# Performance work log

Measured on AMD Instinct MI355X. Metric: run time of the kernel, lower is better.

Reference implementation:

```python
import jax, jax.numpy as jnp
import numpy as np

HEADS = 16
DIM_HEAD = 64

def setup_inputs() -> dict:
    key = jax.random.key(0)
    k1, k2, k3 = jax.random.split(key, 3)
    B, F, N, DIM = 4, 16, 196, 1024
    ntok = 1 + F * N  # cls + frames*patches
    x = jax.random.normal(k1, (B, ntok, DIM), dtype=jnp.float32)
    w_qkv = jax.random.normal(k2, (DIM, 3 * HEADS * DIM_HEAD), dtype=jnp.float32) * (DIM ** -0.5)
    w_out = jax.random.normal(k3, (HEADS * DIM_HEAD, DIM), dtype=jnp.float32) * ((HEADS * DIM_HEAD) ** -0.5)
    return {"x": x, "w_qkv": w_qkv, "w_out": w_out, "f": F}

def _attn(q, k, v):
    # q: [b, i, d], k/v: [b, j, d]
    sim = jnp.einsum('bid,bjd->bij', q, k)
    a = jax.nn.softmax(sim, axis=-1)
    return jnp.einsum('bij,bjd->bid', a, v)

def reference(x, w_qkv, w_out, f):
    B, ntok, dim = x.shape
    h, dh = HEADS, DIM_HEAD
    n = (ntok - 1) // f  # patches per frame
    scale = dh ** -0.5

    qkv = x @ w_qkv  # [B, ntok, 3*h*dh]
    q, k, v = jnp.split(qkv, 3, axis=-1)
    # 'b n (h d) -> (b h) n d'
    def split_heads(t):
        return t.reshape(B, ntok, h, dh).transpose(0, 2, 1, 3).reshape(B * h, ntok, dh)
    q, k, v = split_heads(q) * scale, split_heads(k), split_heads(v)

    cls_q, q_ = q[:, :1], q[:, 1:]
    cls_k, k_ = k[:, :1], k[:, 1:]
    cls_v, v_ = v[:, :1], v[:, 1:]

    # cls token attends to everything
    cls_out = _attn(cls_q, k, v)  # [(b h), 1, d]

    # axial rearrange: '(b h) (f n) d -> (b h f) n d' (spatial attention)
    def to_axial(t):
        return t.reshape(B * h, f, n, dh).reshape(B * h * f, n, dh)
    q_, k_, v_ = map(to_axial, (q_, k_, v_))

    # broadcast cls kv to each frame: 'b () d -> (b r) () d', r = f
    cls_k_r = jnp.repeat(cls_k, f, axis=0)
    cls_v_r = jnp.repeat(cls_v, f, axis=0)
    k_ = jnp.concatenate((cls_k_r, k_), axis=1)  # [(b h f), 1+n, d]
    v_ = jnp.concatenate((cls_v_r, v_), axis=1)

    out = _attn(q_, k_, v_)  # [(b h f), n, d]
    # back: '(b h f) n d -> (b h) (f n) d'
    out = out.reshape(B * h, f * n, dh)
    out = jnp.concatenate((cls_out, out), axis=1)  # [(b h), ntok, d]
    # '(b h) n d -> b n (h d)'
    out = out.reshape(B, h, ntok, dh).transpose(0, 2, 1, 3).reshape(B, ntok, h * dh)
    return out @ w_out
```

## Files before the change

kernel.cpp:

```cpp
#include <hip/hip_runtime.h>
#include <stdint.h>

typedef unsigned short u16;
typedef unsigned int u32;
typedef __attribute__((ext_vector_type(4))) float f32x4;
typedef __attribute__((ext_vector_type(4))) float float4v;
typedef __attribute__((ext_vector_type(8))) short short8;
typedef __attribute__((ext_vector_type(4))) u32 u32x4;
typedef __attribute__((ext_vector_type(4))) u16 u16x4;
typedef __attribute__((ext_vector_type(8))) u16 u16x8;

#define DEV static __device__ __forceinline__

#define NTOK 3137
#define MROWS 12548
#define NHEAD 16
#define DH 64

DEV float bf2f(u16 h){ u32 u = ((u32)h)<<16; float f; __builtin_memcpy(&f,&u,4); return f; }
DEV u16 f2bf(float f){ u32 u; __builtin_memcpy(&u,&f,4); u32 r = u + 0x7FFFu + ((u>>16)&1u); return (u16)(r>>16); }

DEV void gl_lds16(const u16* g, u16* l){
  __builtin_amdgcn_global_load_lds((const __attribute__((address_space(1))) void*)g,
                                   (__attribute__((address_space(3))) void*)l, 16, 0, 0);
}

__global__ __launch_bounds__(256) void cast_bf16_kernel(const float* __restrict__ in,
                                                        u16* __restrict__ out, int n4){
  int i = blockIdx.x*256 + threadIdx.x;
  int stride = gridDim.x*256;
  for(; i < n4; i += stride){
    float4v v = *(const float4v*)(in + (size_t)i*4);
    u16x4 o;
    for(int e=0;e<4;++e) o[e] = f2bf(v[e]);
    *(u16x4*)(out + (size_t)i*4) = o;
  }
}

__global__ void transpose_cast_kernel(const float* __restrict__ in, u16* __restrict__ out,
                                      int R, int C){
  __shared__ float tile[32][33];
  int c0 = blockIdx.x<<5, r0 = blockIdx.y<<5;
  int tx = threadIdx.x, ty = threadIdx.y;
  for(int k=0;k<32;k+=8) tile[ty+k][tx] = in[(size_t)(r0+ty+k)*C + c0+tx];
  __syncthreads();
  for(int k=0;k<32;k+=8) out[(size_t)(c0+ty+k)*R + r0+tx] = f2bf(tile[tx][ty+k]);
}

template<int EPI>
__global__ __launch_bounds__(256) void gemm_kernel(
    const u16* __restrict__ A, const u16* __restrict__ Bt,
    u16* __restrict__ Qb, u16* __restrict__ Kb, u16* __restrict__ Vb,
    float* __restrict__ Out, int Mtot)
{
  __shared__ __align__(16) char smem[EPI==0 ? 34816 : 36864];
  u16* lA = (u16*)smem;
  u16* lB = (u16*)(smem + 8192);
  const int tid = threadIdx.x, lane = tid & 63, wv = tid >> 6;

  const int nwg = gridDim.x, chunk = nwg >> 3, orig = blockIdx.x;
  const int wg = (orig & 7)*chunk + (orig >> 3);
  int bx, by;
  if constexpr(EPI==0){ by = wg/24; bx = wg - by*24; }
  else               { by = wg>>3; bx = wg&7; }

  const int m0 = by<<7, n0 = bx<<7;
  const int wm = (wv>>1)<<6, wn = (wv&1)<<6;
  f32x4 acc[4][4];
  for(int i=0;i<4;++i) for(int j=0;j<4;++j) acc[i][j] = (f32x4){0.f,0.f,0.f,0.f};

  for(int kt=0; kt<32; ++kt){
    const int k0 = kt<<5;
    __syncthreads();
    for(int cc=0; cc<4; ++cc){
      int c = (wv<<2) + cc;
      int row = ((c&7)<<4) + (lane>>2);
      int slot = lane & 3;
      if(c < 8){
        int gr = m0 + row; if(gr >= Mtot) gr = Mtot-1;
        gl_lds16(A + (size_t)gr*1024 + k0 + (slot<<3), lA + (c<<9));
      } else {
        int gr = n0 + row;
        gl_lds16(Bt + (size_t)gr*1024 + k0 + (slot<<3), lB + ((c-8)<<9));
      }
    }
    __syncthreads();
    short8 af[4], bfr[4];
    for(int i=0;i<4;++i){
      int r  = wm + (i<<4) + (lane&15);
      af[i]  = *(const short8*)&lA[(r<<5) + ((lane>>4)<<3)];
      int cn = wn + (i<<4) + (lane&15);
      bfr[i] = *(const short8*)&lB[(cn<<5) + ((lane>>4)<<3)];
    }
    for(int i=0;i<4;++i)
      for(int j=0;j<4;++j)
        acc[i][j] = __builtin_amdgcn_mfma_f32_16x16x32_bf16(af[i], bfr[j], acc[i][j], 0,0,0);
  }

  if constexpr(EPI==0){
    const int which = n0 >> 10;
    const int hbase = (n0 & 1023) >> 6;
    const float sc = (which==0) ? 0.125f : 1.0f;
    u16* dst = (which==0)?Qb:((which==1)?Kb:Vb);
    u16* lC = (u16*)smem;
    __syncthreads();
    for(int i=0;i<4;++i){
      int rb = wm + (i<<4) + ((lane>>4)<<2);
      for(int j=0;j<4;++j){
        int cc = wn + (j<<4) + (lane&15);
        for(int r=0;r<4;++r) lC[(rb+r)*136 + cc] = f2bf(acc[i][j][r]*sc);
      }
    }
    __syncthreads();
    for(int it=0; it<8; ++it){
      int idx = it*256 + tid;
      int row = idx >> 4;
      int half = (idx >> 3) & 1;
      int slot = idx & 7;
      int mm = m0 + row;
      if(mm < Mtot){
        int b = mm / NTOK, tok = mm - b*NTOK;
        u16x8 v = *(const u16x8*)&lC[row*136 + half*64 + slot*8];
        *(u16x8*)(dst + (((size_t)(b*NHEAD + hbase + half)*NTOK + tok)<<6) + slot*8) = v;
      }
    }
  } else {
    float* lF = (float*)smem;
    __syncthreads();
    for(int p=0;p<2;++p){
      if((wv&1)==p){
        for(int i=0;i<4;++i){
          int rb = wm + (i<<4) + ((lane>>4)<<2);
          for(int j=0;j<4;++j){
            int cc = (j<<4) + (lane&15);
            for(int r=0;r<4;++r) lF[(rb+r)*72 + cc] = acc[i][j][r];
          }
        }
      }
      __syncthreads();
      for(int it=0; it<8; ++it){
        int idx = it*256 + tid;
        int row = idx >> 4;
        int slot = idx & 15;
        int mm = m0 + row;
        if(mm < Mtot){
          float4v v = *(const float4v*)&lF[row*72 + slot*4];
          *(float4v*)(Out + (size_t)mm*1024 + n0 + p*64 + slot*4) = v;
        }
      }
      __syncthreads();
    }
  }
}

__global__ __launch_bounds__(256) void cls_partial_kernel(
    const u16* __restrict__ Qb, const u16* __restrict__ Kb, const u16* __restrict__ Vb,
    float* __restrict__ part)
{
  __shared__ float qs[64];
  __shared__ float pbuf[4][64];
  __shared__ float wm[4], wl[4];
  __shared__ float wacc[4][64];
  const int tid = threadIdx.x, lane = tid & 63, wv = tid >> 6;
  const int c = blockIdx.x, bh = blockIdx.y;
  const u16* Kh = Kb + (size_t)bh*NTOK*DH;
  const u16* Vh = Vb + (size_t)bh*NTOK*DH;
  if(tid < 64) qs[tid] = bf2f(Qb[(size_t)bh*NTOK*DH + tid]);
  __syncthreads();

  const int jb = c*256 + wv*64;
  const int j = jb + lane;
  float s = -1e30f;
  if(j < NTOK){
    const u16* kr = Kh + (size_t)j*DH;
    float dot = 0.f;
    for(int t=0;t<8;++t){
      u16x8 kv = *(const u16x8*)(kr + t*8);
      for(int e=0;e<8;++e) dot += bf2f(kv[e]) * qs[t*8+e];
    }
    s = dot;
  }
  float mw = s;
  for(int off=1; off<64; off<<=1) mw = fmaxf(mw, __shfl_xor(mw, off));
  float p = (j < NTOK) ? __expf(s - mw) : 0.f;
  float lw = p;
  for(int off=1; off<64; off<<=1) lw += __shfl_xor(lw, off);
  pbuf[wv][lane] = p;

  float accd = 0.f;
  if(jb < NTOK){
    int nv = NTOK - jb; if(nv > 64) nv = 64;
    for(int jj=0; jj<nv; ++jj)
      accd += pbuf[wv][jj] * bf2f(Vh[(size_t)(jb+jj)*DH + lane]);
  }
  wacc[wv][lane] = accd;
  if(lane==0){ wm[wv]=mw; wl[wv]=lw; }
  __syncthreads();
  if(wv==0){
    float M = fmaxf(fmaxf(wm[0],wm[1]), fmaxf(wm[2],wm[3]));
    float L=0.f, A=0.f;
    for(int wi=0; wi<4; ++wi){
      float e = __expf(wm[wi]-M);
      L += wl[wi]*e; A += wacc[wi][lane]*e;
    }
    float* dst = part + ((size_t)bh*13 + c)*68;
    if(lane==0){ dst[0]=M; dst[1]=L; }
    dst[2+lane] = A;
  }
}

__global__ __launch_bounds__(64) void cls_reduce_kernel(
    const float* __restrict__ part, u16* __restrict__ Abuf)
{
  const int lane = threadIdx.x, bh = blockIdx.x;
  const float* p0 = part + (size_t)bh*13*68;
  float M = -1e30f;
  for(int i=0;i<13;++i) M = fmaxf(M, p0[i*68]);
  float L=0.f, A=0.f;
  for(int i=0;i<13;++i){
    float e = __expf(p0[i*68] - M);
    L += p0[i*68+1]*e;
    A += p0[i*68+2+lane]*e;
  }
  int b = bh>>4, h = bh&15;
  Abuf[(size_t)b*NTOK*1024 + h*DH + lane] = f2bf(A/L);
}

__global__ __launch_bounds__(256) void axial_attn_kernel(
    const u16* __restrict__ Qb, const u16* __restrict__ Kb, const u16* __restrict__ Vb,
    u16* __restrict__ Abuf)
{
  __shared__ u16 lV[64*232];
  __shared__ u16 lP[4*16*232];
  const int tid = threadIdx.x, lane = tid & 63, wv = tid >> 6;
  const int bf = blockIdx.x, bh = bf >> 4, fi = bf & 15;
  const u16* Kh = Kb + (size_t)bh*NTOK*DH;
  const u16* Vh = Vb + (size_t)bh*NTOK*DH;
  const u16* Qh = Qb + (size_t)bh*NTOK*DH;

  for(int c = tid; c < 224*8; c += 256){
    int tok = c >> 3, slot = c & 7;
    u16 vals[8];
    if(tok <= 196){
      size_t row = (tok==0) ? 0 : (size_t)(fi*196 + tok)*DH;
      u16x8 v = *(const u16x8*)(Vh + row + slot*8);
      for(int e=0;e<8;++e) vals[e] = v[e];
    } else {
      for(int e=0;e<8;++e) vals[e] = 0;
    }
    for(int e=0;e<8;++e) lV[(slot*8+e)*232 + tok] = vals[e];
  }
  for(int c = tid; c < 4*16*16; c += 256){
    int w2 = c >> 8, rem = c & 255, row = rem >> 4, cc = rem & 15;
    lP[w2*(16*232) + row*232 + 208 + cc] = 0;
  }
  __syncthreads();

  u16* myP = lP + wv*(16*232);
  const int b_i = bh >> 4, h = bh & 15;

  for(int qt = wv; qt < 13; qt += 4){
    int qr = qt*16 + (lane&15);
    int qrc = qr < 196 ? qr : 195;
    size_t qrow = (size_t)(1 + fi*196 + qrc)*DH;
    short8 qa0 = *(const short8*)(Qh + qrow + ((lane>>4)<<3));
    short8 qa1 = *(const short8*)(Qh + qrow + 32 + ((lane>>4)<<3));

    f32x4 s[13];
    for(int t=0;t<13;++t){
      int tok = t*16 + (lane&15);
      int tokc = tok < 197 ? tok : 196;
      size_t krow = (tokc==0) ? 0 : (size_t)(fi*196 + tokc)*DH;
      short8 b0 = *(const short8*)(Kh + krow + ((lane>>4)<<3));
      short8 b1 = *(const short8*)(Kh + krow + 32 + ((lane>>4)<<3));
      f32x4 z = {0.f,0.f,0.f,0.f};
      z = __builtin_amdgcn_mfma_f32_16x16x32_bf16(qa0, b0, z, 0,0,0);
      z = __builtin_amdgcn_mfma_f32_16x16x32_bf16(qa1, b1, z, 0,0,0);
      s[t] = z;
    }
    int mycol = lane & 15;
    if(192 + mycol >= 197)
      for(int r=0;r<4;++r) s[12][r] = -1e30f;

    f32x4 mx = s[0];
    for(int t=1;t<13;++t) for(int r=0;r<4;++r) mx[r] = fmaxf(mx[r], s[t][r]);
    for(int off=1; off<16; off<<=1)
      for(int r=0;r<4;++r) mx[r] = fmaxf(mx[r], __shfl_xor(mx[r], off));
    f32x4 lsum = {0.f,0.f,0.f,0.f};
    for(int t=0;t<13;++t) for(int r=0;r<4;++r){
      float p = __expf(s[t][r] - mx[r]); s[t][r] = p; lsum[r] += p;
    }
    for(int off=1; off<16; off<<=1)
      for(int r=0;r<4;++r) lsum[r] += __shfl_xor(lsum[r], off);

    for(int t=0;t<13;++t){
      int tok = t*16 + mycol;
      for(int r=0;r<4;++r) myP[(((lane>>4)<<2)+r)*232 + tok] = f2bf(s[t][r]);
    }

    f32x4 o[4] = {{0.f,0.f,0.f,0.f},{0.f,0.f,0.f,0.f},{0.f,0.f,0.f,0.f},{0.f,0.f,0.f,0.f}};
    for(int t2=0;t2<7;++t2){
      short8 a = *(const short8*)&myP[(lane&15)*232 + t2*32 + ((lane>>4)<<3)];
      for(int nd=0;nd<4;++nd){
        short8 b = *(const short8*)&lV[(nd*16 + (lane&15))*232 + t2*32 + ((lane>>4)<<3)];
        o[nd] = __builtin_amdgcn_mfma_f32_16x16x32_bf16(a, b, o[nd], 0,0,0);
      }
    }

    for(int nd=0; nd<4; ++nd){
      int d = nd*16 + (lane&15);
      for(int r=0;r<4;++r){
        int rr = ((lane>>4)<<2) + r;
        myP[rr*72 + d] = f2bf(o[nd][r] / lsum[r]);
      }
    }
    asm volatile("s_waitcnt lgkmcnt(0)" ::: "memory");
    for(int it=0; it<2; ++it){
      int idx = it*64 + lane;
      int row = idx >> 3, slot = idx & 7;
      int ql = qt*16 + row;
      if(ql < 196){
        u16x8 v = *(const u16x8*)&myP[row*72 + slot*8];
        int tok = 1 + fi*196 + ql;
        *(u16x8*)(Abuf + ((size_t)b_i*NTOK + tok)*1024 + h*DH + slot*8) = v;
      }
    }
  }
}

extern "C" void kernel_launch(void* const* d_in, const int* in_sizes, int n_in,
                              void* d_out, int out_size, void* d_ws, size_t ws_size,
                              hipStream_t stream) {
  const float* x     = (const float*)d_in[0];
  const float* wqkv  = (const float*)d_in[1];
  const float* wout  = (const float*)d_in[2];
  float* out = (float*)d_out;
  char* ws = (char*)d_ws;

  u16* xb     = (u16*)(ws);
  u16* Abuf   = xb;
  u16* wqkvT  = (u16*)(ws + 25698304);
  float* clsPart = (float*)(ws + 25698304);
  u16* woutT  = (u16*)(ws + 31989760);
  u16* Qb     = (u16*)(ws + 34086912);
  u16* Kb     = (u16*)(ws + 59785216);
  u16* Vb     = (u16*)(ws + 85483520);

  cast_bf16_kernel<<<dim3(2048), dim3(256), 0, stream>>>(x, xb, (MROWS*1024)/4);
  transpose_cast_kernel<<<dim3(96,32), dim3(32,8), 0, stream>>>(wqkv, wqkvT, 1024, 3072);
  transpose_cast_kernel<<<dim3(32,32), dim3(32,8), 0, stream>>>(wout, woutT, 1024, 1024);

  gemm_kernel<0><<<dim3(2376), dim3(256), 0, stream>>>(xb, wqkvT, Qb, Kb, Vb, nullptr, MROWS);

  cls_partial_kernel<<<dim3(13,64), dim3(256), 0, stream>>>(Qb, Kb, Vb, clsPart);
  cls_reduce_kernel<<<dim3(64), dim3(64), 0, stream>>>(clsPart, Abuf);
  axial_attn_kernel<<<dim3(1024), dim3(256), 0, stream>>>(Qb, Kb, Vb, Abuf);

  gemm_kernel<1><<<dim3(792), dim3(256), 0, stream>>>(Abuf, woutT, nullptr, nullptr, nullptr, out, MROWS);
}
```

Baseline: 236.0 us.

## Replace GEMMs with 256x256 double-buffered swizzled 8-wave MFMA kernel

Both projection GEMMs now use a 256x256 tile kernel with 512 threads, a K step of 64, double-buffered LDS with XOR swizzle, and a hand-scheduled barrier/waitcnt pipeline that overlaps global-to-LDS loads with MFMA phases. The aim is to raise data reuse per tile and hide load latency, which the old single-buffered 128x128 kernel exposed. The epilogues are adapted to write the larger tile in halves or quarters through LDS. The risks are higher register pressure, only one block per CU because of the 128KB LDS footprint, and wasted work on the padded last row tile.

New measurement: 218.7 us. -7.3%, faster.

```diff
diff --git a/kernel.cpp b/kernel.cpp
--- a/kernel.cpp
+++ b/kernel.cpp
@@ -16,6 +16,7 @@
 #define MROWS 12548
 #define NHEAD 16
 #define DH 64
+#define NKT 16
 
 DEV float bf2f(u16 h){ u32 u = ((u32)h)<<16; float f; __builtin_memcpy(&f,&u,4); return f; }
 DEV u16 f2bf(float f){ u32 u; __builtin_memcpy(&u,&f,4); u32 r = u + 0x7FFFu + ((u>>16)&1u); return (u16)(r>>16); }
@@ -24,6 +25,10 @@
   __builtin_amdgcn_global_load_lds((const __attribute__((address_space(1))) void*)g,
                                    (__attribute__((address_space(3))) void*)l, 16, 0, 0);
 }
+
+#define BARRIER()  asm volatile("s_barrier" ::: "memory")
+#define WAIT_LGKM0() asm volatile("s_waitcnt lgkmcnt(0)" ::: "memory")
+#define WAIT_VM(n)  asm volatile("s_waitcnt vmcnt(" #n ")" ::: "memory")
 
 __global__ __launch_bounds__(256) void cast_bf16_kernel(const float* __restrict__ in,
                                                         u16* __restrict__ out, int n4){
@@ -48,54 +53,125 @@
 }
 
 template<int EPI>
-__global__ __launch_bounds__(256) void gemm_kernel(
+__global__ __launch_bounds__(512, 2) void gemm256_kernel(
     const u16* __restrict__ A, const u16* __restrict__ Bt,
     u16* __restrict__ Qb, u16* __restrict__ Kb, u16* __restrict__ Vb,
-    float* __restrict__ Out, int Mtot)
+    float* __restrict__ Out, int Mtot, int tilesx)
 {
-  __shared__ __align__(16) char smem[EPI==0 ? 34816 : 36864];
-  u16* lA = (u16*)smem;
-  u16* lB = (u16*)(smem + 8192);
-  const int tid = threadIdx.x, lane = tid & 63, wv = tid >> 6;
+  __shared__ __align__(16) char smem[131072];
+  const int tid = threadIdx.x, lane = tid & 63, wid = tid >> 6;
+  const int wr = wid >> 2, wc = wid & 3;
 
   const int nwg = gridDim.x, chunk = nwg >> 3, orig = blockIdx.x;
   const int wg = (orig & 7)*chunk + (orig >> 3);
-  int bx, by;
-  if constexpr(EPI==0){ by = wg/24; bx = wg - by*24; }
-  else               { by = wg>>3; bx = wg&7; }
-
-  const int m0 = by<<7, n0 = bx<<7;
-  const int wm = (wv>>1)<<6, wn = (wv&1)<<6;
-  f32x4 acc[4][4];
-  for(int i=0;i<4;++i) for(int j=0;j<4;++j) acc[i][j] = (f32x4){0.f,0.f,0.f,0.f};
-
-  for(int kt=0; kt<32; ++kt){
-    const int k0 = kt<<5;
-    __syncthreads();
-    for(int cc=0; cc<4; ++cc){
-      int c = (wv<<2) + cc;
-      int row = ((c&7)<<4) + (lane>>2);
-      int slot = lane & 3;
-      if(c < 8){
-        int gr = m0 + row; if(gr >= Mtot) gr = Mtot-1;
-        gl_lds16(A + (size_t)gr*1024 + k0 + (slot<<3), lA + (c<<9));
-      } else {
-        int gr = n0 + row;
-        gl_lds16(Bt + (size_t)gr*1024 + k0 + (slot<<3), lB + ((c-8)<<9));
-      }
-    }
-    __syncthreads();
-    short8 af[4], bfr[4];
-    for(int i=0;i<4;++i){
-      int r  = wm + (i<<4) + (lane&15);
-      af[i]  = *(const short8*)&lA[(r<<5) + ((lane>>4)<<3)];
-      int cn = wn + (i<<4) + (lane&15);
-      bfr[i] = *(const short8*)&lB[(cn<<5) + ((lane>>4)<<3)];
-    }
+  const int by = wg / tilesx, bx = wg - by*tilesx;
+  const int m0 = by << 8, n0 = bx << 8;
+
+  f32x4 acc[8][4];
+  #pragma unroll
+  for(int i=0;i<8;++i)
+    #pragma unroll
+    for(int j=0;j<4;++j) acc[i][j] = (f32x4){0.f,0.f,0.f,0.f};
+
+  auto STAGE = [&](int t, int hi){
+    const int bsel = t & 1;
+    char* base = smem + bsel*65536 + ((hi>>1)<<15) + ((hi&1)<<14);
+    const u16* mat = (hi < 2) ? A : Bt;
+    const int rbase = ((hi < 2) ? m0 : n0) + ((hi&1)<<7);
+    #pragma unroll
+    for(int j=0;j<2;++j){
+      int idx = j*512 + tid;
+      int r = idx >> 3;
+      int c2s = ((idx&7)<<4) ^ ((r&7)<<4);
+      int grow = rbase + r;
+      if(hi < 2 && grow >= Mtot) grow = Mtot - 1;
+      const u16* src = mat + (size_t)grow*1024 + t*64 + (c2s>>1);
+      u16* dst = (u16*)(base + j*8192 + wid*1024);
+      gl_lds16(src, dst);
+    }
+  };
+
+  const int rA   = (lane&15)*128;
+  const int csw0 = (((lane>>4)<<4)      ) ^ ((lane&7)<<4);
+  const int csw1 = (((lane>>4)<<4) + 64 ) ^ ((lane&7)<<4);
+
+  auto RDA = [&](int bsel, int i, int kk)->short8 {
+    const char* p = smem + bsel*65536 + (wr<<14) + (i<<4)*128 + rA + (kk ? csw1 : csw0);
+    return *(const short8*)p;
+  };
+  auto RDB = [&](int bsel, int jn, int kk)->short8 {
+    const char* p = smem + bsel*65536 + 32768 + ((wc>>1)<<14)
+                  + (((wc&1)<<6) + (jn<<4))*128 + rA + (kk ? csw1 : csw0);
+    return *(const short8*)p;
+  };
+
+  STAGE(0,0); STAGE(0,1); STAGE(0,2); STAGE(0,3); STAGE(1,0);
+  WAIT_VM(2);
+  BARRIER();
+
+  short8 aR[4][2], b0[2][2], b1[2][2];
+  for(int t=0; t<NKT; ++t){
+    const int bs = t & 1;
+    #pragma unroll
+    for(int i=0;i<4;++i){ aR[i][0]=RDA(bs,i,0); aR[i][1]=RDA(bs,i,1); }
+    #pragma unroll
+    for(int j=0;j<2;++j){ b0[j][0]=RDB(bs,j,0); b0[j][1]=RDB(bs,j,1); }
+    if(t+1<NKT) STAGE(t+1,1);
+    BARRIER(); WAIT_LGKM0();
+    __builtin_amdgcn_s_setprio(1);
+    #pragma unroll
     for(int i=0;i<4;++i)
-      for(int j=0;j<4;++j)
-        acc[i][j] = __builtin_amdgcn_mfma_f32_16x16x32_bf16(af[i], bfr[j], acc[i][j], 0,0,0);
-  }
+      #pragma unroll
+      for(int j=0;j<2;++j){
+        acc[i][j] = __builtin_amdgcn_mfma_f32_16x16x32_bf16(aR[i][0], b0[j][0], acc[i][j], 0,0,0);
+        acc[i][j] = __builtin_amdgcn_mfma_f32_16x16x32_bf16(aR[i][1], b0[j][1], acc[i][j], 0,0,0);
+      }
+    __builtin_amdgcn_s_setprio(0);
+    BARRIER();
+    #pragma unroll
+    for(int j=0;j<2;++j){ b1[j][0]=RDB(bs,2+j,0); b1[j][1]=RDB(bs,2+j,1); }
+    if(t+1<NKT) STAGE(t+1,2);
+    BARRIER(); WAIT_LGKM0();
+    __builtin_amdgcn_s_setprio(1);
+    #pragma unroll
+    for(int i=0;i<4;++i)
+      #pragma unroll
+      for(int j=0;j<2;++j){
+        acc[i][2+j] = __builtin_amdgcn_mfma_f32_16x16x32_bf16(aR[i][0], b1[j][0], acc[i][2+j], 0,0,0);
+        acc[i][2+j] = __builtin_amdgcn_mfma_f32_16x16x32_bf16(aR[i][1], b1[j][1], acc[i][2+j], 0,0,0);
+      }
+    __builtin_amdgcn_s_setprio(0);
+    BARRIER();
+    #pragma unroll
+    for(int i=0;i<4;++i){ aR[i][0]=RDA(bs,4+i,0); aR[i][1]=RDA(bs,4+i,1); }
+    if(t+1<NKT) STAGE(t+1,3);
+    BARRIER(); WAIT_LGKM0();
+    __builtin_amdgcn_s_setprio(1);
+    #pragma unroll
+    for(int i=0;i<4;++i)
+      #pragma unroll
+      for(int j=0;j<2;++j){
+        acc[4+i][2+j] = __builtin_amdgcn_mfma_f32_16x16x32_bf16(aR[i][0], b1[j][0], acc[4+i][2+j], 0,0,0);
+        acc[4+i][2+j] = __builtin_amdgcn_mfma_f32_16x16x32_bf16(aR[i][1], b1[j][1], acc[4+i][2+j], 0,0,0);
+      }
+    __builtin_amdgcn_s_setprio(0);
+    BARRIER();
+    if(t+2<NKT) STAGE(t+2,0);
+    if(t < NKT-2){ WAIT_VM(2); } else { WAIT_VM(0); }
+    BARRIER();
+    __builtin_amdgcn_s_setprio(1);
+    #pragma unroll
+    for(int i=0;i<4;++i)
+      #pragma unroll
+      for(int j=0;j<2;++j){
+        acc[4+i][j] = __builtin_amdgcn_mfma_f32_16x16x32_bf16(aR[i][0], b0[j][0], acc[4+i][j], 0,0,0);
+        acc[4+i][j] = __builtin_amdgcn_mfma_f32_16x16x32_bf16(aR[i][1], b0[j][1], acc[4+i][j], 0,0,0);
+      }
+    __builtin_amdgcn_s_setprio(0);
+    BARRIER();
+  }
+
+  __syncthreads();
 
   if constexpr(EPI==0){
     const int which = n0 >> 10;
@@ -103,49 +179,56 @@
     const float sc = (which==0) ? 0.125f : 1.0f;
     u16* dst = (which==0)?Qb:((which==1)?Kb:Vb);
     u16* lC = (u16*)smem;
-    __syncthreads();
-    for(int i=0;i<4;++i){
-      int rb = wm + (i<<4) + ((lane>>4)<<2);
-      for(int j=0;j<4;++j){
-        int cc = wn + (j<<4) + (lane&15);
-        for(int r=0;r<4;++r) lC[(rb+r)*136 + cc] = f2bf(acc[i][j][r]*sc);
-      }
-    }
-    __syncthreads();
-    for(int it=0; it<8; ++it){
-      int idx = it*256 + tid;
-      int row = idx >> 4;
-      int half = (idx >> 3) & 1;
-      int slot = idx & 7;
-      int mm = m0 + row;
-      if(mm < Mtot){
-        int b = mm / NTOK, tok = mm - b*NTOK;
-        u16x8 v = *(const u16x8*)&lC[row*136 + half*64 + slot*8];
-        *(u16x8*)(dst + (((size_t)(b*NHEAD + hbase + half)*NTOK + tok)<<6) + slot*8) = v;
-      }
+    for(int rh=0; rh<2; ++rh){
+      if(wr == rh){
+        #pragma unroll
+        for(int i=0;i<8;++i){
+          int rr = (i<<4) + ((lane>>4)<<2);
+          #pragma unroll
+          for(int j=0;j<4;++j){
+            int ct = (wc<<6) + (j<<4) + (lane&15);
+            #pragma unroll
+            for(int r=0;r<4;++r) lC[(rr+r)*264 + ct] = f2bf(acc[i][j][r]*sc);
+          }
+        }
+      }
+      __syncthreads();
+      for(int it=0; it<8; ++it){
+        int idx = it*512 + tid;
+        int row = idx >> 5, rest = idx & 31, hh = rest>>3, slot = rest&7;
+        int mm = m0 + rh*128 + row;
+        if(mm < Mtot){
+          int b = mm / NTOK, tok = mm - b*NTOK;
+          u16x8 v = *(const u16x8*)&lC[row*264 + hh*64 + slot*8];
+          *(u16x8*)(dst + (((size_t)(b*NHEAD + hbase + hh)*NTOK + tok)<<6) + slot*8) = v;
+        }
+      }
+      __syncthreads();
     }
   } else {
     float* lF = (float*)smem;
-    __syncthreads();
-    for(int p=0;p<2;++p){
-      if((wv&1)==p){
-        for(int i=0;i<4;++i){
-          int rb = wm + (i<<4) + ((lane>>4)<<2);
+    for(int ph=0; ph<4; ++ph){
+      int rh = ph>>1, ch = ph&1;
+      if(wr==rh && (wc>>1)==ch){
+        #pragma unroll
+        for(int i=0;i<8;++i){
+          int rr = (i<<4) + ((lane>>4)<<2);
+          #pragma unroll
           for(int j=0;j<4;++j){
-            int cc = (j<<4) + (lane&15);
-            for(int r=0;r<4;++r) lF[(rb+r)*72 + cc] = acc[i][j][r];
+            int ct = ((wc&1)<<6) + (j<<4) + (lane&15);
+            #pragma unroll
+            for(int r=0;r<4;++r) lF[(rr+r)*132 + ct] = acc[i][j][r];
           }
         }
       }
       __syncthreads();
       for(int it=0; it<8; ++it){
-        int idx = it*256 + tid;
-        int row = idx >> 4;
-        int slot = idx & 15;
-        int mm = m0 + row;
+        int idx = it*512 + tid;
+        int row = idx >> 5, slot = idx & 31;
+        int mm = m0 + rh*128 + row;
         if(mm < Mtot){
-          float4v v = *(const float4v*)&lF[row*72 + slot*4];
-          *(float4v*)(Out + (size_t)mm*1024 + n0 + p*64 + slot*4) = v;
+          float4v v = *(const float4v*)&lF[row*132 + slot*4];
+          *(float4v*)(Out + (size_t)mm*1024 + n0 + ch*128 + slot*4) = v;
         }
       }
       __syncthreads();
@@ -198,14 +281,14 @@
   __syncthreads();
   if(wv==0){
     float M = fmaxf(fmaxf(wm[0],wm[1]), fmaxf(wm[2],wm[3]));
-    float L=0.f, A=0.f;
+    float L=0.f, Acc=0.f;
     for(int wi=0; wi<4; ++wi){
       float e = __expf(wm[wi]-M);
-      L += wl[wi]*e; A += wacc[wi][lane]*e;
-    }
-    float* dst = part + ((size_t)bh*13 + c)*68;
-    if(lane==0){ dst[0]=M; dst[1]=L; }
-    dst[2+lane] = A;
+      L += wl[wi]*e; Acc += wacc[wi][lane]*e;
+    }
+    float* dstp = part + ((size_t)bh*13 + c)*68;
+    if(lane==0){ dstp[0]=M; dstp[1]=L; }
+    dstp[2+lane] = Acc;
   }
 }
 
@@ -216,14 +299,14 @@
   const float* p0 = part + (size_t)bh*13*68;
   float M = -1e30f;
   for(int i=0;i<13;++i) M = fmaxf(M, p0[i*68]);
-  float L=0.f, A=0.f;
+  float L=0.f, Acc=0.f;
   for(int i=0;i<13;++i){
     float e = __expf(p0[i*68] - M);
     L += p0[i*68+1]*e;
-    A += p0[i*68+2+lane]*e;
+    Acc += p0[i*68+2+lane]*e;
   }
   int b = bh>>4, h = bh&15;
-  Abuf[(size_t)b*NTOK*1024 + h*DH + lane] = f2bf(A/L);
+  Abuf[(size_t)b*NTOK*1024 + h*DH + lane] = f2bf(Acc/L);
 }
 
 __global__ __launch_bounds__(256) void axial_attn_kernel(
@@ -271,11 +354,11 @@
       int tok = t*16 + (lane&15);
       int tokc = tok < 197 ? tok : 196;
       size_t krow = (tokc==0) ? 0 : (size_t)(fi*196 + tokc)*DH;
-      short8 b0 = *(const short8*)(Kh + krow + ((lane>>4)<<3));
-      short8 b1 = *(const short8*)(Kh + krow + 32 + ((lane>>4)<<3));
+      short8 b0v = *(const short8*)(Kh + krow + ((lane>>4)<<3));
+      short8 b1v = *(const short8*)(Kh + krow + 32 + ((lane>>4)<<3));
       f32x4 z = {0.f,0.f,0.f,0.f};
-      z = __builtin_amdgcn_mfma_f32_16x16x32_bf16(qa0, b0, z, 0,0,0);
-      z = __builtin_amdgcn_mfma_f32_16x16x32_bf16(qa1, b1, z, 0,0,0);
+      z = __builtin_amdgcn_mfma_f32_16x16x32_bf16(qa0, b0v, z, 0,0,0);
+      z = __builtin_amdgcn_mfma_f32_16x16x32_bf16(qa1, b1v, z, 0,0,0);
       s[t] = z;
     }
     int mycol = lane & 15;
@@ -350,11 +433,11 @@
   transpose_cast_kernel<<<dim3(96,32), dim3(32,8), 0, stream>>>(wqkv, wqkvT, 1024, 3072);
   transpose_cast_kernel<<<dim3(32,32), dim3(32,8), 0, stream>>>(wout, woutT, 1024, 1024);
 
-  gemm_kernel<0><<<dim3(2376), dim3(256), 0, stream>>>(xb, wqkvT, Qb, Kb, Vb, nullptr, MROWS);
+  gemm256_kernel<0><<<dim3(600), dim3(512), 0, stream>>>(xb, wqkvT, Qb, Kb, Vb, nullptr, MROWS, 12);
 
   cls_partial_kernel<<<dim3(13,64), dim3(256), 0, stream>>>(Qb, Kb, Vb, clsPart);
   cls_reduce_kernel<<<dim3(64), dim3(64), 0, stream>>>(clsPart, Abuf);
   axial_attn_kernel<<<dim3(1024), dim3(256), 0, stream>>>(Qb, Kb, Vb, Abuf);
 
-  gemm_kernel<1><<<dim3(792), dim3(256), 0, stream>>>(Abuf, woutT, nullptr, nullptr, nullptr, out, MROWS);
-}
+  gemm256_kernel<1><<<dim3(200), dim3(512), 0, stream>>>(Abuf, woutT, nullptr, nullptr, nullptr, out, MROWS, 4);
+}
```
